# Kernel optimization log

Hardware: AMD Instinct MI355X
Metric: run time of the kernel (lower is better)

The kernel has to match this reference:

```python
import jax, jax.numpy as jnp
import numpy as np
from jax import lax

K = 3  # kernel size
KK = K * K


def _bilinear_gather(img, ys, xs):
    """img: [C, H, W]; ys, xs: [KK, H, W] float sample coords.
    Returns [C, KK, H, W], zero outside the image (torch DCN zero-pad semantics)."""
    C, H, W = img.shape
    y0 = jnp.floor(ys).astype(jnp.int32)
    x0 = jnp.floor(xs).astype(jnp.int32)
    y1, x1 = y0 + 1, x0 + 1
    wy1 = ys - y0.astype(ys.dtype)
    wx1 = xs - x0.astype(xs.dtype)
    wy0, wx0 = 1.0 - wy1, 1.0 - wx1

    def g(yi, xi):
        valid = ((yi >= 0) & (yi < H) & (xi >= 0) & (xi < W)).astype(img.dtype)
        yc = jnp.clip(yi, 0, H - 1)
        xc = jnp.clip(xi, 0, W - 1)
        return img[:, yc, xc] * valid[None]  # [C, KK, H, W]

    return (wy0 * wx0) * g(y0, x0) + (wy0 * wx1) * g(y0, x1) \
         + (wy1 * wx0) * g(y1, x0) + (wy1 * wx1) * g(y1, x1)


def _df_layer(x, w_off, b_off, w):
    """One DFConv2d (modulated DCN, k=3, s=1, d=1, pad=1, groups=1) + ReLU."""
    B, C, H, W = x.shape
    O = w.shape[0]
    # offset/mask conv (standard 3x3, pad 1, with bias)
    om = lax.conv_general_dilated(x, w_off, (1, 1), [(1, 1), (1, 1)],
                                  dimension_numbers=('NCHW', 'OIHW', 'NCHW'))
    om = om + b_off[None, :, None, None]                     # [B, 27, H, W]
    off = om[:, :2 * KK].reshape(B, KK, 2, H, W)             # (dy, dx) per kernel pt
    mask = jax.nn.sigmoid(om[:, 2 * KK:3 * KK])              # [B, KK, H, W]

    ki, kj = jnp.meshgrid(jnp.arange(K), jnp.arange(K), indexing='ij')
    # base sampling grid: y = h - pad + i*dil = h + i - 1
    base_y = jnp.arange(H, dtype=x.dtype)[None, :, None] + (ki.reshape(KK, 1, 1).astype(x.dtype) - 1.0)
    base_x = jnp.arange(W, dtype=x.dtype)[None, None, :] + (kj.reshape(KK, 1, 1).astype(x.dtype) - 1.0)
    ys = base_y + off[:, :, 0]                               # [B, KK, H, W]
    xs = base_x + off[:, :, 1]

    sampled = jax.vmap(_bilinear_gather)(x, ys, xs)          # [B, C, KK, H, W]
    out = jnp.einsum('oik,bikhw->bohw', w.reshape(O, C, KK), sampled * mask[:, None])
    return jax.nn.relu(out)


def setup_inputs() -> dict:
    key = jax.random.key(0)
    ks = jax.random.split(key, 7)
    s = 0.05
    return {
        'x': jax.random.normal(ks[0], (2, 256, 96, 96), dtype=jnp.float32),
        'w_off0': jax.random.normal(ks[1], (27, 256, 3, 3), dtype=jnp.float32) * s,
        'b_off0': jnp.zeros((27,), dtype=jnp.float32),
        'w0': jax.random.normal(ks[2], (256, 256, 3, 3), dtype=jnp.float32) * s,
        'w_off1': jax.random.normal(ks[3], (27, 256, 3, 3), dtype=jnp.float32) * s,
        'b_off1': jnp.zeros((27,), dtype=jnp.float32),
        'w1': jax.random.normal(ks[4], (256, 256, 3, 3), dtype=jnp.float32) * s,
    }


def reference(x, w_off0, b_off0, w0, w_off1, b_off1, w1):
    h = _df_layer(x, w_off0, b_off0, w0)
    h = _df_layer(h, w_off1, b_off1, w1)
    return h
```

## Files before the change

### kernel.cpp

```cpp
#include <hip/hip_runtime.h>
#include <cstdint>
#include <cstddef>


#define KTOT 2304
#define PXB  9216

typedef __attribute__((ext_vector_type(8))) short bf16x8;
typedef __attribute__((ext_vector_type(4))) float f32x4;

static __device__ __forceinline__ unsigned short f2bf(float f) {
    union { float f; unsigned int u; } v; v.f = f;
    unsigned int r = (v.u + 0x7FFFu + ((v.u >> 16) & 1u)) >> 16;
    return (unsigned short)r;
}
static __device__ __forceinline__ float bf2f(unsigned short h) {
    union { unsigned int u; float f; } v; v.u = ((unsigned int)h) << 16;
    return v.f;
}
static __device__ __forceinline__ void unpack8(uint4 u, float* f) {
    union { unsigned int u; float f; } t;
    t.u = u.x << 16;         f[0] = t.f;
    t.u = u.x & 0xffff0000u; f[1] = t.f;
    t.u = u.y << 16;         f[2] = t.f;
    t.u = u.y & 0xffff0000u; f[3] = t.f;
    t.u = u.z << 16;         f[4] = t.f;
    t.u = u.z & 0xffff0000u; f[5] = t.f;
    t.u = u.w << 16;         f[6] = t.f;
    t.u = u.w & 0xffff0000u; f[7] = t.f;
}

__global__ __launch_bounds__(256) void transpose_kernel(const float* __restrict__ in,
                                                        unsigned short* __restrict__ outH,
                                                        unsigned short* __restrict__ outL) {
    __shared__ float tile[64][65];
    const int hw0 = blockIdx.x * 64;
    const int c0  = blockIdx.y * 64;
    const int b   = blockIdx.z;
    const int lx  = threadIdx.x & 63;
    const int ly  = threadIdx.x >> 6;
#pragma unroll
    for (int i = 0; i < 16; ++i) {
        int cl = ly + i * 4;
        tile[cl][lx] = in[(size_t)(b * 256 + c0 + cl) * PXB + hw0 + lx];
    }
    __syncthreads();
#pragma unroll
    for (int i = 0; i < 16; ++i) {
        int hwl = ly + i * 4;
        float v = tile[lx][hwl];
        size_t oi = ((size_t)b * PXB + hw0 + hwl) * 256 + c0 + lx;
        unsigned short hi = f2bf(v);
        outH[oi] = hi;
        outL[oi] = f2bf(v - bf2f(hi));
    }
}

__global__ __launch_bounds__(256) void prep_w_kernel(const float* __restrict__ w,
                                                     unsigned short* __restrict__ wA) {
    int idx = blockIdx.x * 256 + threadIdx.x;
    int o = idx / KTOT;
    int k = idx - o * KTOT;
    int kk = k >> 8;
    int c  = k & 255;
    wA[idx] = f2bf(w[o * KTOT + c * 9 + kk]);
}

__global__ __launch_bounds__(256) void prep_woff_kernel(const float* __restrict__ w,
                                                        unsigned short* __restrict__ wH,
                                                        unsigned short* __restrict__ wL) {
    int idx = blockIdx.x * 256 + threadIdx.x;
    int o = idx / KTOT;
    int k = idx - o * KTOT;
    int kk = k >> 8;
    int c  = k & 255;
    float f = (o < 27) ? w[o * KTOT + c * 9 + kk] : 0.0f;
    unsigned short hi = f2bf(f);
    wH[idx] = hi;
    wL[idx] = f2bf(f - bf2f(hi));
}

__global__ __launch_bounds__(512) void offconv_fused(const unsigned short* __restrict__ xH,
                                                     const unsigned short* __restrict__ xL,
                                                     const unsigned short* __restrict__ AH,
                                                     const unsigned short* __restrict__ AL,
                                                     const float* __restrict__ bias,
                                                     float* __restrict__ om) {
    __shared__ __attribute__((aligned(16))) unsigned short AsH[2][32 * 72];
    __shared__ __attribute__((aligned(16))) unsigned short AsL[2][32 * 72];
    __shared__ __attribute__((aligned(16))) unsigned short BsH[2][64 * 72];
    __shared__ __attribute__((aligned(16))) unsigned short BsL[2][64 * 72];

    const int tid  = threadIdx.x;
    const int kg   = tid >> 8;
    const int tl   = tid & 255;
    const int lane = tid & 63;
    const int wq   = (tid >> 6) & 3;
    const int quad = lane >> 4, l16 = lane & 15;
    const int g    = blockIdx.x;
    const int nb   = (g & 7) * 36 + (g >> 3);
    const int n0   = nb * 64;
    const int b    = n0 / PXB;
    const int hw0  = n0 - b * PXB;

    f32x4 acc[2];
#pragma unroll
    for (int mt = 0; mt < 2; ++mt) acc[mt] = (f32x4)0.0f;

    const int arow = tl >> 3, akg = tl & 7;

    uint4 pAH, pAL, pBH0, pBL0, pBH1, pBL1;
    auto pf = [&](int it) {
        const int kt = kg * 18 + it;
        const int kk = kt >> 2, c0 = (kt & 3) * 64;
        const int dy = kk / 3 - 1, dx = kk - (kk / 3) * 3 - 1;
        size_t ai = (size_t)arow * KTOT + kt * 64 + akg * 8;
        pAH = *(const uint4*)&AH[ai];
        pAL = *(const uint4*)&AL[ai];
#pragma unroll
        for (int i = 0; i < 2; ++i) {
            int task = i * 256 + tl;
            int px = task >> 3, cg = task & 7;
            int hw = hw0 + px;
            int h = hw / 96, w = hw - h * 96;
            int y = h + dy, x = w + dx;
            uint4 hv = make_uint4(0u, 0u, 0u, 0u), lv = make_uint4(0u, 0u, 0u, 0u);
            if (((unsigned)y < 96u) && ((unsigned)x < 96u)) {
                size_t bi = ((size_t)b * PXB + y * 96 + x) * 256 + c0 + cg * 8;
                hv = *(const uint4*)&xH[bi];
                lv = *(const uint4*)&xL[bi];
            }
            if (i == 0) { pBH0 = hv; pBL0 = lv; } else { pBH1 = hv; pBL1 = lv; }
        }
    };
    pf(0);

    for (int it = 0; it < 18; ++it) {
        __syncthreads();
        *(uint4*)&AsH[kg][arow * 72 + akg * 8] = pAH;
        *(uint4*)&AsL[kg][arow * 72 + akg * 8] = pAL;
        {
            int px = tl >> 3, cg = tl & 7;
            *(uint4*)&BsH[kg][px * 72 + cg * 8] = pBH0;
            *(uint4*)&BsL[kg][px * 72 + cg * 8] = pBL0;
        }
        {
            int task = 256 + tl;
            int px = task >> 3, cg = task & 7;
            *(uint4*)&BsH[kg][px * 72 + cg * 8] = pBH1;
            *(uint4*)&BsL[kg][px * 72 + cg * 8] = pBL1;
        }
        if (it < 17) pf(it + 1);
        __syncthreads();
#pragma unroll
        for (int ks = 0; ks < 2; ++ks) {
            bf16x8 ah[2], al[2], bh, bl;
#pragma unroll
            for (int mt = 0; mt < 2; ++mt) {
                ah[mt] = *(const bf16x8*)&AsH[kg][(mt * 16 + l16) * 72 + ks * 32 + quad * 8];
                al[mt] = *(const bf16x8*)&AsL[kg][(mt * 16 + l16) * 72 + ks * 32 + quad * 8];
            }
            bh = *(const bf16x8*)&BsH[kg][(wq * 16 + l16) * 72 + ks * 32 + quad * 8];
            bl = *(const bf16x8*)&BsL[kg][(wq * 16 + l16) * 72 + ks * 32 + quad * 8];
#pragma unroll
            for (int mt = 0; mt < 2; ++mt) {
                acc[mt] = __builtin_amdgcn_mfma_f32_16x16x32_bf16(ah[mt], bh, acc[mt], 0, 0, 0);
                acc[mt] = __builtin_amdgcn_mfma_f32_16x16x32_bf16(ah[mt], bl, acc[mt], 0, 0, 0);
                acc[mt] = __builtin_amdgcn_mfma_f32_16x16x32_bf16(al[mt], bh, acc[mt], 0, 0, 0);
            }
        }
    }

    float* red = (float*)BsH;
    __syncthreads();
    if (kg == 1) {
#pragma unroll
        for (int mt = 0; mt < 2; ++mt)
#pragma unroll
            for (int r = 0; r < 4; ++r)
                red[wq * 512 + mt * 256 + quad * 64 + r * 16 + l16] = acc[mt][r];
    }
    __syncthreads();
    if (kg == 0) {
#pragma unroll
        for (int mt = 0; mt < 2; ++mt)
#pragma unroll
            for (int r = 0; r < 4; ++r) {
                float v = acc[mt][r] + red[wq * 512 + mt * 256 + quad * 64 + r * 16 + l16];
                int m = mt * 16 + quad * 4 + r;
                int n = wq * 16 + l16;
                if (m < 27)
                    om[(size_t)(b * 27 + m) * PXB + hw0 + n] = v + bias[m];
            }
    }
}

__global__ __launch_bounds__(512) void dfconv_v5(const unsigned short* __restrict__ xB,
                                                 const float* __restrict__ om,
                                                 const unsigned short* __restrict__ A,
                                                 float* __restrict__ out,
                                                 unsigned short* __restrict__ outH,
                                                 unsigned short* __restrict__ outL,
                                                 int out_mode) {
    __shared__ __attribute__((aligned(16))) char smem[71360];
    unsigned short* BsD  = (unsigned short*)(smem + 32768);
    unsigned short* goff = (unsigned short*)(smem + 55808);
    float*          gwt  = (float*)(smem + 60992);

    const int tid  = threadIdx.x;
    const int wv   = tid >> 6;
    const int lane = tid & 63;
    const int quad = lane >> 4, l16 = lane & 15;
    const int g    = blockIdx.x;
    const int nb   = (g & 7) * 32 + (g >> 3);
    const int b    = nb >> 7;
    const int hw0  = (nb & 127) * 72;

    for (int task = tid; task < 648; task += 512) {
        int px = task / 9;
        int kk = task - px * 9;
        int hw = hw0 + px;
        int h = hw / 96, w = hw - h * 96;
        const float* omp = om + (size_t)b * 27 * PXB + hw;
        float dyv = omp[(size_t)(2 * kk) * PXB];
        float dxv = omp[(size_t)(2 * kk + 1) * PXB];
        float mv  = omp[(size_t)(18 + kk) * PXB];
        float mk  = 1.0f / (1.0f + __expf(-mv));

        float ys = (float)(h + (kk / 3) - 1) + dyv;
        float xs = (float)(w + (kk - (kk / 3) * 3) - 1) + dxv;
        float fy = floorf(ys), fx = floorf(xs);
        int iy = (int)fy, ix = (int)fx;
        float wy1 = ys - fy, wx1 = xs - fx;
        float wy0 = 1.0f - wy1, wx0 = 1.0f - wx1;
        bool yv0 = (unsigned)iy < 96u, yv1 = (unsigned)(iy + 1) < 96u;
        bool xv0 = (unsigned)ix < 96u, xv1 = (unsigned)(ix + 1) < 96u;
        int y0 = min(max(iy, 0), 95),     y1 = min(max(iy + 1, 0), 95);
        int x0 = min(max(ix, 0), 95),     x1 = min(max(ix + 1, 0), 95);
        int gg = task * 4;
        goff[gg + 0] = (unsigned short)(y0 * 96 + x0);
        goff[gg + 1] = (unsigned short)(y0 * 96 + x1);
        goff[gg + 2] = (unsigned short)(y1 * 96 + x0);
        goff[gg + 3] = (unsigned short)(y1 * 96 + x1);
        gwt[gg + 0] = (yv0 && xv0) ? mk * wy0 * wx0 : 0.0f;
        gwt[gg + 1] = (yv0 && xv1) ? mk * wy0 * wx1 : 0.0f;
        gwt[gg + 2] = (yv1 && xv0) ? mk * wy1 * wx0 : 0.0f;
        gwt[gg + 3] = (yv1 && xv1) ? mk * wy1 * wx1 : 0.0f;
    }
    for (int i = tid; i < 576; i += 512) {
        int buf = i / 288, rem = i - buf * 288;
        int row = 72 + rem / 36, col2 = (rem - (rem / 36) * 36) * 2;
        *(unsigned int*)&BsD[buf * 5760 + row * 72 + col2] = 0u;
    }
    __syncthreads();

    const int px  = tid >> 3;
    const int cg  = tid & 7;
    const int px2 = 64 + (tid >> 3);
    const int cg2 = tid & 7;
    const unsigned short* xbase  = xB + (size_t)b * PXB * 256 + cg * 8;
    const unsigned short* xbase2 = xB + (size_t)b * PXB * 256 + cg2 * 8;

    const int arl = lane >> 3;
    const int akg = (lane & 7) ^ arl;

    f32x4 acc[2][5];
#pragma unroll
    for (int mt = 0; mt < 2; ++mt)
#pragma unroll
        for (int nt = 0; nt < 5; ++nt) acc[mt][nt] = (f32x4)0.0f;

    auto dmaA = [&](int kt) {
#pragma unroll
        for (int s = 0; s < 4; ++s) {
            const unsigned short* src =
                A + (size_t)(wv * 32 + s * 8 + arl) * KTOT + kt * 64 + akg * 8;
            char* dst = smem + wv * 4096 + s * 1024;
            __builtin_amdgcn_global_load_lds(
                (const __attribute__((address_space(1))) unsigned int*)src,
                (__attribute__((address_space(3))) unsigned int*)dst, 16, 0, 0);
        }
    };

    dmaA(0);
    {
        int gg = (px * 9 + 0) * 4;
        ushort4 o4 = *(const ushort4*)&goff[gg];
        float4 wt = *(const float4*)&gwt[gg];
        uint4 u0 = *(const uint4*)(xbase + (size_t)o4.x * 256);
        uint4 u1 = *(const uint4*)(xbase + (size_t)o4.y * 256);
        uint4 u2 = *(const uint4*)(xbase + (size_t)o4.z * 256);
        uint4 u3 = *(const uint4*)(xbase + (size_t)o4.w * 256);
        float f0[8], f1[8], f2[8], f3[8];
        unpack8(u0, f0); unpack8(u1, f1); unpack8(u2, f2); unpack8(u3, f3);
        unsigned short res[8];
#pragma unroll
        for (int j = 0; j < 8; ++j)
            res[j] = f2bf(wt.x * f0[j] + wt.y * f1[j] + wt.z * f2[j] + wt.w * f3[j]);
        *(uint4*)&BsD[px * 72 + cg * 8] = *(uint4*)res;
    }
    if (tid < 64) {
        int gg = (px2 * 9 + 0) * 4;
        ushort4 o4 = *(const ushort4*)&goff[gg];
        float4 wt = *(const float4*)&gwt[gg];
        uint4 u0 = *(const uint4*)(xbase2 + (size_t)o4.x * 256);
        uint4 u1 = *(const uint4*)(xbase2 + (size_t)o4.y * 256);
        uint4 u2 = *(const uint4*)(xbase2 + (size_t)o4.z * 256);
        uint4 u3 = *(const uint4*)(xbase2 + (size_t)o4.w * 256);
        float f0[8], f1[8], f2[8], f3[8];
        unpack8(u0, f0); unpack8(u1, f1); unpack8(u2, f2); unpack8(u3, f3);
        unsigned short res[8];
#pragma unroll
        for (int j = 0; j < 8; ++j)
            res[j] = f2bf(wt.x * f0[j] + wt.y * f1[j] + wt.z * f2[j] + wt.w * f3[j]);
        *(uint4*)&BsD[px2 * 72 + cg2 * 8] = *(uint4*)res;
    }
    __syncthreads();

    for (int r = 0; r < 36; ++r) {
        const int cur = r & 1;

        uint4 cc0, cc1, cc2, cc3; float4 wt;
        uint4 dd0, dd1, dd2, dd3; float4 wt2;
        if (r < 35) {
            const int ktn = r + 1, tap = ktn >> 2, c0 = (ktn & 3) * 64;
            {
                int gg = (px * 9 + tap) * 4;
                ushort4 o4 = *(const ushort4*)&goff[gg];
                wt = *(const float4*)&gwt[gg];
                const unsigned short* cb = xbase + c0;
                cc0 = *(const uint4*)(cb + (size_t)o4.x * 256);
                cc1 = *(const uint4*)(cb + (size_t)o4.y * 256);
                cc2 = *(const uint4*)(cb + (size_t)o4.z * 256);
                cc3 = *(const uint4*)(cb + (size_t)o4.w * 256);
            }
            if (tid < 64) {
                int gg = (px2 * 9 + tap) * 4;
                ushort4 o4 = *(const ushort4*)&goff[gg];
                wt2 = *(const float4*)&gwt[gg];
                const unsigned short* cb = xbase2 + c0;
                dd0 = *(const uint4*)(cb + (size_t)o4.x * 256);
                dd1 = *(const uint4*)(cb + (size_t)o4.y * 256);
                dd2 = *(const uint4*)(cb + (size_t)o4.z * 256);
                dd3 = *(const uint4*)(cb + (size_t)o4.w * 256);
            }
        }

        bf16x8 af00, af01, af10, af11;
        {
            const char* Ac = smem + wv * 4096;
            const int sw0 = ((quad ^ (l16 & 7)) * 16);
            const int sw1 = (((4 + quad) ^ (l16 & 7)) * 16);
            af00 = *(const bf16x8*)(Ac + l16 * 128 + sw0);
            af01 = *(const bf16x8*)(Ac + (16 + l16) * 128 + sw0);
            af10 = *(const bf16x8*)(Ac + l16 * 128 + sw1);
            af11 = *(const bf16x8*)(Ac + (16 + l16) * 128 + sw1);
        }
        asm volatile("s_waitcnt lgkmcnt(0)" ::: "memory");
        __builtin_amdgcn_sched_barrier(0);

        if (r < 35) dmaA(r + 1);

        {
            const unsigned short* Br = BsD + cur * 5760;
#pragma unroll
            for (int nt = 0; nt < 5; ++nt) {
                bf16x8 b0 = *(const bf16x8*)&Br[(nt * 16 + l16) * 72 + quad * 8];
                acc[0][nt] = __builtin_amdgcn_mfma_f32_16x16x32_bf16(af00, b0, acc[0][nt], 0, 0, 0);
                acc[1][nt] = __builtin_amdgcn_mfma_f32_16x16x32_bf16(af01, b0, acc[1][nt], 0, 0, 0);
            }
#pragma unroll
            for (int nt = 0; nt < 5; ++nt) {
                bf16x8 b1 = *(const bf16x8*)&Br[(nt * 16 + l16) * 72 + 32 + quad * 8];
                acc[0][nt] = __builtin_amdgcn_mfma_f32_16x16x32_bf16(af10, b1, acc[0][nt], 0, 0, 0);
                acc[1][nt] = __builtin_amdgcn_mfma_f32_16x16x32_bf16(af11, b1, acc[1][nt], 0, 0, 0);
            }
        }

        if (r < 35) {
            unsigned short* Bw = BsD + (cur ^ 1) * 5760;
            {
                float f0[8], f1[8], f2[8], f3[8];
                unpack8(cc0, f0); unpack8(cc1, f1); unpack8(cc2, f2); unpack8(cc3, f3);
                unsigned short res[8];
#pragma unroll
                for (int j = 0; j < 8; ++j)
                    res[j] = f2bf(wt.x * f0[j] + wt.y * f1[j] + wt.z * f2[j] + wt.w * f3[j]);
                *(uint4*)&Bw[px * 72 + cg * 8] = *(uint4*)res;
            }
            if (tid < 64) {
                float f0[8], f1[8], f2[8], f3[8];
                unpack8(dd0, f0); unpack8(dd1, f1); unpack8(dd2, f2); unpack8(dd3, f3);
                unsigned short res[8];
#pragma unroll
                for (int j = 0; j < 8; ++j)
                    res[j] = f2bf(wt2.x * f0[j] + wt2.y * f1[j] + wt2.z * f2[j] + wt2.w * f3[j]);
                *(uint4*)&Bw[px2 * 72 + cg2 * 8] = *(uint4*)res;
            }
        }

        __syncthreads();
    }

    float* tileS = (float*)smem;
    if (out_mode == 0) {
#pragma unroll
        for (int pass = 0; pass < 4; ++pass) {
            if ((wv >> 1) == pass) {
#pragma unroll
                for (int mt = 0; mt < 2; ++mt)
#pragma unroll
                    for (int nt = 0; nt < 5; ++nt)
#pragma unroll
                        for (int rr = 0; rr < 4; ++rr) {
                            int ml = (wv & 1) * 32 + mt * 16 + quad * 4 + rr;
                            int n  = nt * 16 + l16;
                            tileS[ml * 80 + n] = fmaxf(acc[mt][nt][rr], 0.0f);
                        }
            }
            __syncthreads();
#pragma unroll
            for (int j = 0; j < 3; ++j) {
                int idx = j * 512 + tid;
                if (idx < 1152) {
                    int row = idx / 18, q = idx - row * 18;
                    *(float4*)&out[(size_t)(b * 256 + pass * 64 + row) * PXB + hw0 + q * 4] =
                        *(const float4*)&tileS[row * 80 + q * 4];
                }
            }
            __syncthreads();
        }
    } else {
#pragma unroll
        for (int pass = 0; pass < 5; ++pass) {
#pragma unroll
            for (int mt = 0; mt < 2; ++mt) {
                f32x4 v = acc[mt][pass];
                v[0] = fmaxf(v[0], 0.f); v[1] = fmaxf(v[1], 0.f);
                v[2] = fmaxf(v[2], 0.f); v[3] = fmaxf(v[3], 0.f);
                *(f32x4*)&tileS[l16 * 264 + wv * 32 + mt * 16 + quad * 4] = v;
            }
            __syncthreads();
            const int cnt = (pass < 4) ? 1024 : 512;
#pragma unroll
            for (int j = 0; j < 2; ++j) {
                int idx = j * 512 + tid;
                if (idx < cnt) {
                    int pxl = idx >> 6, ln = idx & 63;
                    float4 v = *(const float4*)&tileS[pxl * 264 + ln * 4];
                    size_t oi = ((size_t)b * PXB + hw0 + pass * 16 + pxl) * 256 + ln * 4;
                    unsigned short hv[4], lv[4];
#pragma unroll
                    for (int e = 0; e < 4; ++e) {
                        float fe = (e == 0) ? v.x : (e == 1) ? v.y : (e == 2) ? v.z : v.w;
                        hv[e] = f2bf(fe);
                        lv[e] = f2bf(fe - bf2f(hv[e]));
                    }
                    *(ushort4*)&outH[oi] = *(ushort4*)hv;
                    *(ushort4*)&outL[oi] = *(ushort4*)lv;
                }
            }
            __syncthreads();
        }
    }
}

extern "C" void kernel_launch(void* const* d_in, const int* in_sizes, int n_in,
                              void* d_out, int out_size, void* d_ws, size_t ws_size,
                              hipStream_t stream) {
    const float* x     = (const float*)d_in[0];
    const float* woff0 = (const float*)d_in[1];
    const float* boff0 = (const float*)d_in[2];
    const float* w0    = (const float*)d_in[3];
    const float* woff1 = (const float*)d_in[4];
    const float* boff1 = (const float*)d_in[5];
    const float* w1    = (const float*)d_in[6];
    float* out = (float*)d_out;

    char* p = (char*)d_ws;
    float* om  = (float*)p;  p += (size_t)2 * 27 * PXB * 4;
    unsigned short* xh  = (unsigned short*)p; p += (size_t)2 * 256 * PXB * 2;
    unsigned short* xl  = (unsigned short*)p; p += (size_t)2 * 256 * PXB * 2;
    unsigned short* h1h = (unsigned short*)p; p += (size_t)2 * 256 * PXB * 2;
    unsigned short* h1l = (unsigned short*)p; p += (size_t)2 * 256 * PXB * 2;
    unsigned short* wA0 = (unsigned short*)p; p += (size_t)256 * KTOT * 2;
    unsigned short* wA1 = (unsigned short*)p; p += (size_t)256 * KTOT * 2;
    unsigned short* wH0 = (unsigned short*)p; p += (size_t)32 * KTOT * 2;
    unsigned short* wL0 = (unsigned short*)p; p += (size_t)32 * KTOT * 2;
    unsigned short* wH1 = (unsigned short*)p; p += (size_t)32 * KTOT * 2;
    unsigned short* wL1 = (unsigned short*)p; p += (size_t)32 * KTOT * 2;

    hipLaunchKernelGGL(transpose_kernel, dim3(PXB / 64, 4, 2), dim3(256), 0, stream, x, xh, xl);
    hipLaunchKernelGGL(prep_w_kernel, dim3(256 * KTOT / 256), dim3(256), 0, stream, w0, wA0);
    hipLaunchKernelGGL(prep_w_kernel, dim3(256 * KTOT / 256), dim3(256), 0, stream, w1, wA1);
    hipLaunchKernelGGL(prep_woff_kernel, dim3(32 * KTOT / 256), dim3(256), 0, stream, woff0, wH0, wL0);
    hipLaunchKernelGGL(prep_woff_kernel, dim3(32 * KTOT / 256), dim3(256), 0, stream, woff1, wH1, wL1);

    hipLaunchKernelGGL(offconv_fused, dim3(288), dim3(512), 0, stream, xh, xl, wH0, wL0, boff0, om);
    hipLaunchKernelGGL(dfconv_v5, dim3(256), dim3(512), 0, stream, xh, om, wA0,
                       (float*)nullptr, h1h, h1l, 1);

    hipLaunchKernelGGL(offconv_fused, dim3(288), dim3(512), 0, stream, h1h, h1l, wH1, wL1, boff1, om);
    hipLaunchKernelGGL(dfconv_v5, dim3(256), dim3(512), 0, stream, h1h, om, wA1,
                       out, (unsigned short*)nullptr, (unsigned short*)nullptr, 0);
}
```

Measured before the change: 274.6 us.

## Double-buffer weight tiles and prefetch gathers two stages ahead in dfconv

The deformable-conv GEMM kernel now keeps two LDS buffers for the weight (A) tiles, so the DMA for the next k-step no longer has to wait for the current step's A fragments to be read. The bilinear gather loads are issued two iterations ahead, with explicit vmcnt waits and raw s_barrier in place of __syncthreads. The goal is to hide global-memory latency of both the gather and the weight loads behind the MFMA work. In exchange, shared memory per block grows to about 104 KB and register pressure rises from the extra prefetch registers. The hand-counted vmcnt values are fragile if the compiler reorders or splits the loads.

Measured after the change: 258.1 us. 6.0% less time.

```diff
diff --git a/kernel.cpp b/kernel.cpp
--- a/kernel.cpp
+++ b/kernel.cpp
@@ -195,17 +195,17 @@
     }
 }
 
-__global__ __launch_bounds__(512) void dfconv_v5(const unsigned short* __restrict__ xB,
+__global__ __launch_bounds__(512) void dfconv_v6(const unsigned short* __restrict__ xB,
                                                  const float* __restrict__ om,
                                                  const unsigned short* __restrict__ A,
                                                  float* __restrict__ out,
                                                  unsigned short* __restrict__ outH,
                                                  unsigned short* __restrict__ outL,
                                                  int out_mode) {
-    __shared__ __attribute__((aligned(16))) char smem[71360];
-    unsigned short* BsD  = (unsigned short*)(smem + 32768);
-    unsigned short* goff = (unsigned short*)(smem + 55808);
-    float*          gwt  = (float*)(smem + 60992);
+    __shared__ __attribute__((aligned(16))) char smem[104128];
+    unsigned short* BsD  = (unsigned short*)(smem + 65536);
+    unsigned short* goff = (unsigned short*)(smem + 88576);
+    float*          gwt  = (float*)(smem + 93760);
 
     const int tid  = threadIdx.x;
     const int wv   = tid >> 6;
@@ -257,9 +257,7 @@
     const int px  = tid >> 3;
     const int cg  = tid & 7;
     const int px2 = 64 + (tid >> 3);
-    const int cg2 = tid & 7;
     const unsigned short* xbase  = xB + (size_t)b * PXB * 256 + cg * 8;
-    const unsigned short* xbase2 = xB + (size_t)b * PXB * 256 + cg2 * 8;
 
     const int arl = lane >> 3;
     const int akg = (lane & 7) ^ arl;
@@ -270,98 +268,89 @@
 #pragma unroll
         for (int nt = 0; nt < 5; ++nt) acc[mt][nt] = (f32x4)0.0f;
 
-    auto dmaA = [&](int kt) {
+    auto dmaA = [&](int kt, int buf) {
 #pragma unroll
         for (int s = 0; s < 4; ++s) {
             const unsigned short* src =
                 A + (size_t)(wv * 32 + s * 8 + arl) * KTOT + kt * 64 + akg * 8;
-            char* dst = smem + wv * 4096 + s * 1024;
+            char* dst = smem + buf * 32768 + wv * 4096 + s * 1024;
             __builtin_amdgcn_global_load_lds(
                 (const __attribute__((address_space(1))) unsigned int*)src,
                 (__attribute__((address_space(3))) unsigned int*)dst, 16, 0, 0);
         }
     };
-
-    dmaA(0);
-    {
-        int gg = (px * 9 + 0) * 4;
+    auto loadC = [&](int kt, uint4& c0r, uint4& c1r, uint4& c2r, uint4& c3r,
+                     float4& wtr, int pxl) {
+        const int tap = kt >> 2, cb0 = (kt & 3) * 64;
+        int gg = (pxl * 9 + tap) * 4;
         ushort4 o4 = *(const ushort4*)&goff[gg];
-        float4 wt = *(const float4*)&gwt[gg];
-        uint4 u0 = *(const uint4*)(xbase + (size_t)o4.x * 256);
-        uint4 u1 = *(const uint4*)(xbase + (size_t)o4.y * 256);
-        uint4 u2 = *(const uint4*)(xbase + (size_t)o4.z * 256);
-        uint4 u3 = *(const uint4*)(xbase + (size_t)o4.w * 256);
+        wtr = *(const float4*)&gwt[gg];
+        const unsigned short* cb = xbase + cb0;
+        c0r = *(const uint4*)(cb + (size_t)o4.x * 256);
+        c1r = *(const uint4*)(cb + (size_t)o4.y * 256);
+        c2r = *(const uint4*)(cb + (size_t)o4.z * 256);
+        c3r = *(const uint4*)(cb + (size_t)o4.w * 256);
+    };
+    auto interpC = [&](uint4 c0r, uint4 c1r, uint4 c2r, uint4 c3r, float4 wtr,
+                       unsigned short* Bw, int pxl) {
         float f0[8], f1[8], f2[8], f3[8];
-        unpack8(u0, f0); unpack8(u1, f1); unpack8(u2, f2); unpack8(u3, f3);
+        unpack8(c0r, f0); unpack8(c1r, f1); unpack8(c2r, f2); unpack8(c3r, f3);
         unsigned short res[8];
 #pragma unroll
         for (int j = 0; j < 8; ++j)
-            res[j] = f2bf(wt.x * f0[j] + wt.y * f1[j] + wt.z * f2[j] + wt.w * f3[j]);
-        *(uint4*)&BsD[px * 72 + cg * 8] = *(uint4*)res;
-    }
-    if (tid < 64) {
-        int gg = (px2 * 9 + 0) * 4;
-        ushort4 o4 = *(const ushort4*)&goff[gg];
-        float4 wt = *(const float4*)&gwt[gg];
-        uint4 u0 = *(const uint4*)(xbase2 + (size_t)o4.x * 256);
-        uint4 u1 = *(const uint4*)(xbase2 + (size_t)o4.y * 256);
-        uint4 u2 = *(const uint4*)(xbase2 + (size_t)o4.z * 256);
-        uint4 u3 = *(const uint4*)(xbase2 + (size_t)o4.w * 256);
-        float f0[8], f1[8], f2[8], f3[8];
-        unpack8(u0, f0); unpack8(u1, f1); unpack8(u2, f2); unpack8(u3, f3);
-        unsigned short res[8];
-#pragma unroll
-        for (int j = 0; j < 8; ++j)
-            res[j] = f2bf(wt.x * f0[j] + wt.y * f1[j] + wt.z * f2[j] + wt.w * f3[j]);
-        *(uint4*)&BsD[px2 * 72 + cg2 * 8] = *(uint4*)res;
-    }
-    __syncthreads();
+            res[j] = f2bf(wtr.x * f0[j] + wtr.y * f1[j] + wtr.z * f2[j] + wtr.w * f3[j]);
+        *(uint4*)&Bw[pxl * 72 + cg * 8] = *(uint4*)res;
+    };
+
+    uint4 cc0, cc1, cc2, cc3; float4 cwt;
+    uint4 nn0, nn1, nn2, nn3; float4 nwt;
+    uint4 dc0, dc1, dc2, dc3; float4 dwt;
+    uint4 dn0, dn1, dn2, dn3; float4 dnwt;
+    loadC(0, cc0, cc1, cc2, cc3, cwt, px);
+    if (tid < 64) loadC(0, dc0, dc1, dc2, dc3, dwt, px2);
+    loadC(1, nn0, nn1, nn2, nn3, nwt, px);
+    if (tid < 64) loadC(1, dn0, dn1, dn2, dn3, dnwt, px2);
+    dmaA(0, 0);
+    __builtin_amdgcn_sched_barrier(0);
+    if (wv == 0) { asm volatile("s_waitcnt vmcnt(12)" ::: "memory"); }
+    else         { asm volatile("s_waitcnt vmcnt(8)"  ::: "memory"); }
+    __builtin_amdgcn_sched_barrier(0);
+    interpC(cc0, cc1, cc2, cc3, cwt, BsD, px);
+    if (tid < 64) interpC(dc0, dc1, dc2, dc3, dwt, BsD, px2);
+    cc0 = nn0; cc1 = nn1; cc2 = nn2; cc3 = nn3; cwt = nwt;
+    if (tid < 64) { dc0 = dn0; dc1 = dn1; dc2 = dn2; dc3 = dn3; dwt = dnwt; }
+    asm volatile("s_waitcnt lgkmcnt(0)" ::: "memory");
+    __builtin_amdgcn_sched_barrier(0);
+    __builtin_amdgcn_s_barrier();
 
     for (int r = 0; r < 36; ++r) {
         const int cur = r & 1;
 
-        uint4 cc0, cc1, cc2, cc3; float4 wt;
-        uint4 dd0, dd1, dd2, dd3; float4 wt2;
-        if (r < 35) {
-            const int ktn = r + 1, tap = ktn >> 2, c0 = (ktn & 3) * 64;
-            {
-                int gg = (px * 9 + tap) * 4;
-                ushort4 o4 = *(const ushort4*)&goff[gg];
-                wt = *(const float4*)&gwt[gg];
-                const unsigned short* cb = xbase + c0;
-                cc0 = *(const uint4*)(cb + (size_t)o4.x * 256);
-                cc1 = *(const uint4*)(cb + (size_t)o4.y * 256);
-                cc2 = *(const uint4*)(cb + (size_t)o4.z * 256);
-                cc3 = *(const uint4*)(cb + (size_t)o4.w * 256);
-            }
-            if (tid < 64) {
-                int gg = (px2 * 9 + tap) * 4;
-                ushort4 o4 = *(const ushort4*)&goff[gg];
-                wt2 = *(const float4*)&gwt[gg];
-                const unsigned short* cb = xbase2 + c0;
-                dd0 = *(const uint4*)(cb + (size_t)o4.x * 256);
-                dd1 = *(const uint4*)(cb + (size_t)o4.y * 256);
-                dd2 = *(const uint4*)(cb + (size_t)o4.z * 256);
-                dd3 = *(const uint4*)(cb + (size_t)o4.w * 256);
-            }
-        }
-
-        bf16x8 af00, af01, af10, af11;
+        if (r <= 33) {
+            loadC(r + 2, nn0, nn1, nn2, nn3, nwt, px);
+            if (tid < 64) loadC(r + 2, dn0, dn1, dn2, dn3, dnwt, px2);
+        }
+        if (r <= 34) dmaA(r + 1, cur ^ 1);
+
+        __builtin_amdgcn_sched_barrier(0);
+        if (r <= 33) {
+            if (wv == 0) { asm volatile("s_waitcnt vmcnt(12)" ::: "memory"); }
+            else         { asm volatile("s_waitcnt vmcnt(8)"  ::: "memory"); }
+        } else if (r == 34) {
+            asm volatile("s_waitcnt vmcnt(4)" ::: "memory");
+        } else {
+            asm volatile("s_waitcnt vmcnt(0)" ::: "memory");
+        }
+        __builtin_amdgcn_sched_barrier(0);
+
         {
-            const char* Ac = smem + wv * 4096;
+            const char* Ac = smem + cur * 32768 + wv * 4096;
             const int sw0 = ((quad ^ (l16 & 7)) * 16);
             const int sw1 = (((4 + quad) ^ (l16 & 7)) * 16);
-            af00 = *(const bf16x8*)(Ac + l16 * 128 + sw0);
-            af01 = *(const bf16x8*)(Ac + (16 + l16) * 128 + sw0);
-            af10 = *(const bf16x8*)(Ac + l16 * 128 + sw1);
-            af11 = *(const bf16x8*)(Ac + (16 + l16) * 128 + sw1);
-        }
-        asm volatile("s_waitcnt lgkmcnt(0)" ::: "memory");
-        __builtin_amdgcn_sched_barrier(0);
-
-        if (r < 35) dmaA(r + 1);
-
-        {
+            bf16x8 af00 = *(const bf16x8*)(Ac + l16 * 128 + sw0);
+            bf16x8 af01 = *(const bf16x8*)(Ac + (16 + l16) * 128 + sw0);
+            bf16x8 af10 = *(const bf16x8*)(Ac + l16 * 128 + sw1);
+            bf16x8 af11 = *(const bf16x8*)(Ac + (16 + l16) * 128 + sw1);
             const unsigned short* Br = BsD + cur * 5760;
 #pragma unroll
             for (int nt = 0; nt < 5; ++nt) {
@@ -377,30 +366,21 @@
             }
         }
 
-        if (r < 35) {
+        if (r <= 34) {
             unsigned short* Bw = BsD + (cur ^ 1) * 5760;
-            {
-                float f0[8], f1[8], f2[8], f3[8];
-                unpack8(cc0, f0); unpack8(cc1, f1); unpack8(cc2, f2); unpack8(cc3, f3);
-                unsigned short res[8];
-#pragma unroll
-                for (int j = 0; j < 8; ++j)
-                    res[j] = f2bf(wt.x * f0[j] + wt.y * f1[j] + wt.z * f2[j] + wt.w * f3[j]);
-                *(uint4*)&Bw[px * 72 + cg * 8] = *(uint4*)res;
-            }
-            if (tid < 64) {
-                float f0[8], f1[8], f2[8], f3[8];
-                unpack8(dd0, f0); unpack8(dd1, f1); unpack8(dd2, f2); unpack8(dd3, f3);
-                unsigned short res[8];
-#pragma unroll
-                for (int j = 0; j < 8; ++j)
-                    res[j] = f2bf(wt2.x * f0[j] + wt2.y * f1[j] + wt2.z * f2[j] + wt2.w * f3[j]);
-                *(uint4*)&Bw[px2 * 72 + cg2 * 8] = *(uint4*)res;
-            }
-        }
-
-        __syncthreads();
-    }
+            interpC(cc0, cc1, cc2, cc3, cwt, Bw, px);
+            if (tid < 64) interpC(dc0, dc1, dc2, dc3, dwt, Bw, px2);
+            cc0 = nn0; cc1 = nn1; cc2 = nn2; cc3 = nn3; cwt = nwt;
+            if (tid < 64) { dc0 = dn0; dc1 = dn1; dc2 = dn2; dc3 = dn3; dwt = dnwt; }
+        }
+
+        asm volatile("s_waitcnt lgkmcnt(0)" ::: "memory");
+        __builtin_amdgcn_sched_barrier(0);
+        __builtin_amdgcn_s_barrier();
+    }
+
+    asm volatile("s_waitcnt vmcnt(0) lgkmcnt(0)" ::: "memory");
+    __syncthreads();
 
     float* tileS = (float*)smem;
     if (out_mode == 0) {
@@ -497,10 +477,10 @@
     hipLaunchKernelGGL(prep_woff_kernel, dim3(32 * KTOT / 256), dim3(256), 0, stream, woff1, wH1, wL1);
 
     hipLaunchKernelGGL(offconv_fused, dim3(288), dim3(512), 0, stream, xh, xl, wH0, wL0, boff0, om);
-    hipLaunchKernelGGL(dfconv_v5, dim3(256), dim3(512), 0, stream, xh, om, wA0,
+    hipLaunchKernelGGL(dfconv_v6, dim3(256), dim3(512), 0, stream, xh, om, wA0,
                        (float*)nullptr, h1h, h1l, 1);
 
     hipLaunchKernelGGL(offconv_fused, dim3(288), dim3(512), 0, stream, h1h, h1l, wH1, wL1, boff1, om);
-    hipLaunchKernelGGL(dfconv_v5, dim3(256), dim3(512), 0, stream, h1h, om, wA1,
+    hipLaunchKernelGGL(dfconv_v6, dim3(256), dim3(512), 0, stream, h1h, om, wA1,
                        out, (unsigned short*)nullptr, (unsigned short*)nullptr, 0);
 }
```
